# Kernel tuning notes

Hardware: AMD Instinct MI355X
Metric: run time of the kernel (lower is better)

## Reference

```python
import jax, jax.numpy as jnp
import numpy as np

NEG_INF = jnp.float32(-9e15)

def gat_layer(x, adj_mask, W, a, alpha):
    # x: [N, F_in]; W: [H, F_in, F_out]; a: [H, 2*F_out]; adj_mask: [N, N] bool
    H, _, O = W.shape
    h = jnp.einsum('nf,hfo->hno', x, W)            # [H, N, O]
    a_src, a_dst = a[:, :O], a[:, O:]              # [H, O] each
    e_src = jnp.einsum('hno,ho->hn', h, a_src)     # [H, N]
    e_dst = jnp.einsum('hno,ho->hn', h, a_dst)     # [H, N]
    e = jax.nn.leaky_relu(e_src[:, :, None] + e_dst[:, None, :], negative_slope=alpha)
    e = jnp.where(adj_mask[None, :, :], e, NEG_INF)  # mask non-edges
    attn = jax.nn.softmax(e, axis=-1)              # [H, N, N]
    out = jnp.einsum('hnm,hmo->hno', attn, h)      # [H, N, O]
    return out.mean(axis=0)                        # average heads -> [N, O]

def setup_inputs() -> dict:
    key = jax.random.key(0)
    ks = jax.random.split(key, 6)
    N, F_IN, F_HID, F_CLS, H = 4096, 512, 256, 16, 4
    x = jax.random.normal(ks[0], (N, F_IN), dtype=jnp.float32)
    adj = jax.random.randint(ks[1], (N, N), 0, 2, dtype=jnp.int32)
    W1 = jax.random.normal(ks[2], (H, F_IN, F_HID), dtype=jnp.float32) * 0.05
    a1 = jax.random.normal(ks[3], (H, 2 * F_HID), dtype=jnp.float32) * 0.05
    W2 = jax.random.normal(ks[4], (1, F_HID, F_CLS), dtype=jnp.float32) * 0.05
    a2 = jax.random.normal(ks[5], (1, 2 * F_CLS), dtype=jnp.float32) * 0.05
    return {"x": x, "adj": adj, "W1": W1, "a1": a1, "W2": W2, "a2": a2}

def reference(x, adj, W1, a1, W2, a2):
    alpha = 0.2
    adj_mask = adj > 0
    h = jax.nn.relu(gat_layer(x, adj_mask, W1, a1, alpha))        # layer1 + ReLU
    out = gat_layer(h, adj_mask, W2, a2, alpha)                    # layer2
    return jax.nn.log_softmax(out, axis=1)                         # [N, nclass]
```

## Files before the change

### kernel.cpp

```cpp
#include <hip/hip_runtime.h>
#include <stdint.h>

#define N_NODES 4096
#define F_IN    512
#define F_HID   256
#define F_CLS   16
#define NHEAD   4
#define ALPHA   0.2f

typedef __attribute__((ext_vector_type(8))) short short8;
typedef __attribute__((ext_vector_type(4))) float f32x4;

__device__ __forceinline__ float bf2f(unsigned short h) {
    unsigned u = ((unsigned)h) << 16; float f; __builtin_memcpy(&f, &u, 4); return f;
}
__device__ __forceinline__ unsigned short f2bf(float f) {
    unsigned u; __builtin_memcpy(&u, &f, 4);
    u += 0x7fffu + ((u >> 16) & 1u);
    return (unsigned short)(u >> 16);
}
__device__ __forceinline__ float lo_bf(unsigned u) { u <<= 16;          float f; __builtin_memcpy(&f,&u,4); return f; }
__device__ __forceinline__ float hi_bf(unsigned u) { u &= 0xffff0000u;  float f; __builtin_memcpy(&f,&u,4); return f; }

__device__ __forceinline__ void async_cp16(void* lds, const void* g) {
    __builtin_amdgcn_global_load_lds(
        (const __attribute__((address_space(1))) unsigned int*)g,
        (__attribute__((address_space(3))) unsigned int*)lds,
        16, 0, 0);
}

__global__ __launch_bounds__(256) void k_bitmask(const int* __restrict__ adj,
                                                 unsigned long long* __restrict__ bm) {
    int wv = threadIdx.x >> 6, lane = threadIdx.x & 63;
    int idx0 = blockIdx.x * 1024 + wv * 256;
    const int* p = adj + idx0 + lane;
    unsigned long long m0 = __ballot(p[0]   > 0);
    unsigned long long m1 = __ballot(p[64]  > 0);
    unsigned long long m2 = __ballot(p[128] > 0);
    unsigned long long m3 = __ballot(p[192] > 0);
    if (lane == 0) {
        int w = idx0 >> 6;
        bm[w] = m0; bm[w+1] = m1; bm[w+2] = m2; bm[w+3] = m3;
    }
}

__global__ __launch_bounds__(256) void k_convert(const float* __restrict__ x,
                                                 const float* __restrict__ W1,
                                                 const float* __restrict__ W2,
                                                 unsigned short* __restrict__ xb,
                                                 unsigned short* __restrict__ W1t,
                                                 float* __restrict__ W2t) {
    int tid = blockIdx.x * 256 + threadIdx.x;
    const int NXV = (N_NODES * F_IN) / 8;
    const int NW1 = NHEAD * 64 * F_HID;
    if (tid < NXV) {
        float4 a = *(const float4*)&x[tid * 8];
        float4 b = *(const float4*)&x[tid * 8 + 4];
        uint4 w;
        w.x = (unsigned)f2bf(a.x) | ((unsigned)f2bf(a.y) << 16);
        w.y = (unsigned)f2bf(a.z) | ((unsigned)f2bf(a.w) << 16);
        w.z = (unsigned)f2bf(b.x) | ((unsigned)f2bf(b.y) << 16);
        w.w = (unsigned)f2bf(b.z) | ((unsigned)f2bf(b.w) << 16);
        *(uint4*)&xb[tid * 8] = w;
    } else if (tid < NXV + NW1) {
        int j = tid - NXV;
        int o = j & 255, f8 = (j >> 8) & 63, h = j >> 14;
        float v[8];
        #pragma unroll
        for (int k = 0; k < 8; ++k)
            v[k] = W1[(size_t)(h * F_IN + f8 * 8 + k) * F_HID + o];
        uint4 w;
        w.x = (unsigned)f2bf(v[0]) | ((unsigned)f2bf(v[1]) << 16);
        w.y = (unsigned)f2bf(v[2]) | ((unsigned)f2bf(v[3]) << 16);
        w.z = (unsigned)f2bf(v[4]) | ((unsigned)f2bf(v[5]) << 16);
        w.w = (unsigned)f2bf(v[6]) | ((unsigned)f2bf(v[7]) << 16);
        *(uint4*)&W1t[(size_t)(h * F_HID + o) * F_IN + f8 * 8] = w;
    } else {
        int j = tid - NXV - NW1;
        if (j < F_HID * F_CLS) {
            int o = j >> 4, c = j & 15;
            W2t[c * F_HID + o] = W2[j];
        }
    }
}

__global__ __launch_bounds__(256, 4) void k_gemm1(const unsigned short* __restrict__ xb,
                                                  const unsigned short* __restrict__ W1t,
                                                  const float* __restrict__ a1,
                                                  unsigned short* __restrict__ h1t,
                                                  float* __restrict__ es1,
                                                  float* __restrict__ ed1) {
    __shared__ unsigned short Ald[2][64 * 32];
    __shared__ unsigned short Bld[2][128 * 32];
    const int t = threadIdx.x;
    const int lane = t & 63, wv = t >> 6, quad = lane >> 4, l15 = lane & 15;
    const int wn = wv & 1, wo = wv >> 1;
    const int n0 = blockIdx.x * 128;
    const int mo0 = blockIdx.y * 64;
    const int h = blockIdx.z;

    {
        int chunk = wv * 64 + lane, row = chunk >> 2, ch = lane & 3;
        async_cp16(&Ald[0][wv * 512], W1t + (size_t)(h * F_HID + mo0 + row) * F_IN + ch * 8);
        #pragma unroll
        for (int ps = 0; ps < 2; ++ps) {
            int c2 = (wv * 2 + ps) * 64 + lane, r2 = c2 >> 2;
            async_cp16(&Bld[0][(wv * 2 + ps) * 512], xb + (size_t)(n0 + r2) * F_IN + ch * 8);
        }
    }
    f32x4 acc[2][4] = {};
    for (int it = 0; it < 16; ++it) {
        const int cur = it & 1;
        __syncthreads();
        if (it + 1 < 16) {
            const int k2 = (it + 1) * 32;
            int chunk = wv * 64 + lane, row = chunk >> 2, ch = lane & 3;
            async_cp16(&Ald[1 - cur][wv * 512], W1t + (size_t)(h * F_HID + mo0 + row) * F_IN + k2 + ch * 8);
            #pragma unroll
            for (int ps = 0; ps < 2; ++ps) {
                int c2 = (wv * 2 + ps) * 64 + lane, r2 = c2 >> 2;
                async_cp16(&Bld[1 - cur][(wv * 2 + ps) * 512], xb + (size_t)(n0 + r2) * F_IN + k2 + ch * 8);
            }
        }
        short8 bf[4];
        #pragma unroll
        for (int ni = 0; ni < 4; ++ni)
            bf[ni] = *(const short8*)&Bld[cur][(wn * 64 + ni * 16 + l15) * 32 + quad * 8];
        #pragma unroll
        for (int mi = 0; mi < 2; ++mi) {
            short8 af = *(const short8*)&Ald[cur][(wo * 32 + mi * 16 + l15) * 32 + quad * 8];
            #pragma unroll
            for (int ni = 0; ni < 4; ++ni)
                acc[mi][ni] = __builtin_amdgcn_mfma_f32_16x16x32_bf16(af, bf[ni], acc[mi][ni], 0, 0, 0);
        }
    }
    #pragma unroll
    for (int mi = 0; mi < 2; ++mi)
      #pragma unroll
      for (int ni = 0; ni < 4; ++ni)
        #pragma unroll
        for (int rg = 0; rg < 4; ++rg) {
            int o = mo0 + wo * 32 + mi * 16 + quad * 4 + rg;
            int n = n0 + wn * 64 + ni * 16 + l15;
            h1t[(size_t)(h * F_HID + o) * N_NODES + n] = f2bf(acc[mi][ni][rg]);
        }
    float esp[4] = {}, edp[4] = {};
    #pragma unroll
    for (int mi = 0; mi < 2; ++mi)
      #pragma unroll
      for (int rg = 0; rg < 4; ++rg) {
        int o = mo0 + wo * 32 + mi * 16 + quad * 4 + rg;
        float a1s = a1[h * 2 * F_HID + o];
        float a1d = a1[h * 2 * F_HID + F_HID + o];
        #pragma unroll
        for (int ni = 0; ni < 4; ++ni) {
            esp[ni] += acc[mi][ni][rg] * a1s;
            edp[ni] += acc[mi][ni][rg] * a1d;
        }
      }
    #pragma unroll
    for (int ni = 0; ni < 4; ++ni) {
        esp[ni] += __shfl_xor(esp[ni], 16, 64); esp[ni] += __shfl_xor(esp[ni], 32, 64);
        edp[ni] += __shfl_xor(edp[ni], 16, 64); edp[ni] += __shfl_xor(edp[ni], 32, 64);
    }
    if (quad == 0) {
        #pragma unroll
        for (int ni = 0; ni < 4; ++ni) {
            int n = n0 + wn * 64 + ni * 16 + l15;
            atomicAdd(&es1[h * N_NODES + n], esp[ni]);
            atomicAdd(&ed1[h * N_NODES + n], edp[ni]);
        }
    }
}

__global__ __launch_bounds__(512, 4) void k_attn1(const unsigned short* __restrict__ h1t,
                                                  const float* __restrict__ es1,
                                                  const float* __restrict__ ed1,
                                                  const unsigned char* __restrict__ bmb,
                                                  unsigned short* __restrict__ C1p,
                                                  float* __restrict__ l1p) {
    __shared__ unsigned short Bld[2][256 * 32];
    const int t = threadIdx.x;
    const int lane = t & 63, wv = t >> 6, quad = lane >> 4, l15 = lane & 15;
    const int wvo = wv & 1, wvm = wv >> 1;
    const int m0 = blockIdx.x * 128;
    const int h = blockIdx.y;
    const int kz = blockIdx.z;
    const int mb0 = kz * 1024;

    int m_r0 = m0 + wvm * 32 + l15;
    int m_r1 = m_r0 + 16;
    float esr0 = es1[h * N_NODES + m_r0];
    float esr1 = es1[h * N_NODES + m_r1];
    const unsigned char* bp0 = bmb + (size_t)m_r0 * (N_NODES / 8);
    const unsigned char* bp1 = bmb + (size_t)m_r1 * (N_NODES / 8);
    const float* edb = ed1 + h * N_NODES;

    {
        int ch = lane & 3;
        #pragma unroll
        for (int ps = 0; ps < 2; ++ps) {
            int row = ((wv * 2 + ps) * 64 + lane) >> 2;
            async_cp16(&Bld[0][(wv * 2 + ps) * 512], h1t + (size_t)(h * F_HID + row) * N_NODES + mb0 + ch * 8);
        }
    }
    f32x4 acc[8][2] = {};
    float lsum0 = 0.f, lsum1 = 0.f;
    for (int it = 0; it < 32; ++it) {
        const int cur = it & 1;
        const int mb = mb0 + it * 32;
        __syncthreads();
        if (it + 1 < 32) {
            int ch = lane & 3;
            #pragma unroll
            for (int ps = 0; ps < 2; ++ps) {
                int row = ((wv * 2 + ps) * 64 + lane) >> 2;
                async_cp16(&Bld[1 - cur][(wv * 2 + ps) * 512],
                           h1t + (size_t)(h * F_HID + row) * N_NODES + mb + 32 + ch * 8);
            }
        }
        float4 e0 = *(const float4*)&edb[mb + quad * 8];
        float4 e1v = *(const float4*)&edb[mb + quad * 8 + 4];
        float ev[8] = {e0.x, e0.y, e0.z, e0.w, e1v.x, e1v.y, e1v.z, e1v.w};
        unsigned bb0 = bp0[(mb >> 3) + quad];
        unsigned bb1 = bp1[(mb >> 3) + quad];
        short8 bfrag0, bfrag1;
        #pragma unroll
        for (int j = 0; j < 8; ++j) {
            float s0 = esr0 + ev[j]; s0 = fmaxf(s0, ALPHA * s0);
            float p0 = ((bb0 >> j) & 1u) ? __expf(s0) : 0.f;
            lsum0 += p0; bfrag0[j] = (short)f2bf(p0);
            float s1 = esr1 + ev[j]; s1 = fmaxf(s1, ALPHA * s1);
            float p1 = ((bb1 >> j) & 1u) ? __expf(s1) : 0.f;
            lsum1 += p1; bfrag1[j] = (short)f2bf(p1);
        }
        #pragma unroll
        for (int mi = 0; mi < 8; ++mi) {
            short8 af = *(const short8*)&Bld[cur][(wvo * 128 + mi * 16 + l15) * 32 + quad * 8];
            acc[mi][0] = __builtin_amdgcn_mfma_f32_16x16x32_bf16(af, bfrag0, acc[mi][0], 0, 0, 0);
            acc[mi][1] = __builtin_amdgcn_mfma_f32_16x16x32_bf16(af, bfrag1, acc[mi][1], 0, 0, 0);
        }
    }
    lsum0 += __shfl_xor(lsum0, 16, 64); lsum0 += __shfl_xor(lsum0, 32, 64);
    lsum1 += __shfl_xor(lsum1, 16, 64); lsum1 += __shfl_xor(lsum1, 32, 64);
    if (quad == 0 && wvo == 0) {
        l1p[(size_t)(kz * NHEAD + h) * N_NODES + m_r0] = lsum0;
        l1p[(size_t)(kz * NHEAD + h) * N_NODES + m_r1] = lsum1;
    }
    unsigned short* Cb = C1p + (size_t)(kz * NHEAD + h) * N_NODES * F_HID;
    #pragma unroll
    for (int mi = 0; mi < 8; ++mi)
      #pragma unroll
      for (int ni = 0; ni < 2; ++ni) {
        int o0 = wvo * 128 + mi * 16 + quad * 4;
        int m = (ni == 0) ? m_r0 : m_r1;
        uint2 uu;
        uu.x = (unsigned)f2bf(acc[mi][ni][0]) | ((unsigned)f2bf(acc[mi][ni][1]) << 16);
        uu.y = (unsigned)f2bf(acc[mi][ni][2]) | ((unsigned)f2bf(acc[mi][ni][3]) << 16);
        *(uint2*)&Cb[(size_t)m * F_HID + o0] = uu;
      }
}

__global__ __launch_bounds__(256) void k_reduce1(const unsigned short* __restrict__ C1p,
                                                 const float* __restrict__ l1p,
                                                 unsigned short* __restrict__ h2) {
    int t = threadIdx.x;
    int og = t & 31, nl = t >> 5;
    int n = blockIdx.x * 8 + nl;
    float acc8[8] = {};
    #pragma unroll
    for (int h = 0; h < NHEAD; ++h) {
        float den = 0.f, num[8] = {};
        #pragma unroll
        for (int kz = 0; kz < 4; ++kz) {
            den += l1p[(size_t)(kz * NHEAD + h) * N_NODES + n];
            uint4 u = *(const uint4*)&C1p[((size_t)(kz * NHEAD + h) * N_NODES + n) * F_HID + og * 8];
            num[0] += lo_bf(u.x); num[1] += hi_bf(u.x);
            num[2] += lo_bf(u.y); num[3] += hi_bf(u.y);
            num[4] += lo_bf(u.z); num[5] += hi_bf(u.z);
            num[6] += lo_bf(u.w); num[7] += hi_bf(u.w);
        }
        float rinv = 1.f / fmaxf(den, 1e-30f);
        #pragma unroll
        for (int j = 0; j < 8; ++j) acc8[j] += num[j] * rinv;
    }
    uint4 w;
    unsigned short b[8];
    #pragma unroll
    for (int j = 0; j < 8; ++j) b[j] = f2bf(fmaxf(acc8[j] * 0.25f, 0.f));
    w.x = (unsigned)b[0] | ((unsigned)b[1] << 16);
    w.y = (unsigned)b[2] | ((unsigned)b[3] << 16);
    w.z = (unsigned)b[4] | ((unsigned)b[5] << 16);
    w.w = (unsigned)b[6] | ((unsigned)b[7] << 16);
    *(uint4*)&h2[(size_t)n * F_HID + og * 8] = w;
}

__global__ __launch_bounds__(256) void k_h2w(const unsigned short* __restrict__ h2,
                                             const float* __restrict__ W2t,
                                             const float* __restrict__ a2,
                                             unsigned short* __restrict__ h2wt,
                                             float* __restrict__ es2, float* __restrict__ ed2) {
    int t = threadIdx.x;
    int c = t & 15, nl = t >> 4;
    int n = blockIdx.x * 16 + nl;
    const unsigned short* hrow = h2 + (size_t)n * F_HID;
    const float* wrow = W2t + c * F_HID;
    float dot = 0.f;
    for (int o = 0; o < F_HID; o += 8) {
        uint4 hu = *(const uint4*)&hrow[o];
        float4 w0 = *(const float4*)&wrow[o];
        float4 w1 = *(const float4*)&wrow[o + 4];
        dot += lo_bf(hu.x)*w0.x + hi_bf(hu.x)*w0.y + lo_bf(hu.y)*w0.z + hi_bf(hu.y)*w0.w;
        dot += lo_bf(hu.z)*w1.x + hi_bf(hu.z)*w1.y + lo_bf(hu.w)*w1.z + hi_bf(hu.w)*w1.w;
    }
    h2wt[(size_t)c * N_NODES + n] = f2bf(dot);
    float es = dot * a2[c];
    float ed = dot * a2[F_CLS + c];
    #pragma unroll
    for (int off = 1; off < 16; off <<= 1) {
        es += __shfl_xor(es, off, 64);
        ed += __shfl_xor(ed, off, 64);
    }
    if (c == 0) { es2[n] = es; ed2[n] = ed; }
}

__global__ __launch_bounds__(256, 4) void k_attn2(const unsigned short* __restrict__ h2wt,
                                                  const float* __restrict__ es2,
                                                  const float* __restrict__ ed2,
                                                  const unsigned char* __restrict__ bmb,
                                                  float* __restrict__ out2p,
                                                  float* __restrict__ l2p) {
    const int t = threadIdx.x;
    const int lane = t & 63, wv = t >> 6, quad = lane >> 4, l15 = lane & 15;
    const int m0 = blockIdx.x * 64;
    const int ks = blockIdx.y;
    const int m_r = m0 + wv * 16 + l15;
    const float esr = es2[m_r];
    const unsigned char* bp = bmb + (size_t)m_r * (N_NODES / 8);

    f32x4 acc = {};
    float lsum = 0.f;
    for (int it = 0; it < 16; ++it) {
        const int mb = ks * 512 + it * 32;
        float4 e0 = *(const float4*)&ed2[mb + quad * 8];
        float4 e1v = *(const float4*)&ed2[mb + quad * 8 + 4];
        float ev[8] = {e0.x, e0.y, e0.z, e0.w, e1v.x, e1v.y, e1v.z, e1v.w};
        unsigned bb = bp[(mb >> 3) + quad];
        short8 afrag;
        #pragma unroll
        for (int j = 0; j < 8; ++j) {
            float s = esr + ev[j]; s = fmaxf(s, ALPHA * s);
            float p = ((bb >> j) & 1u) ? __expf(s) : 0.f;
            lsum += p; afrag[j] = (short)f2bf(p);
        }
        short8 bfr = *(const short8*)&h2wt[(size_t)l15 * N_NODES + mb + quad * 8];
        acc = __builtin_amdgcn_mfma_f32_16x16x32_bf16(afrag, bfr, acc, 0, 0, 0);
    }
    lsum += __shfl_xor(lsum, 16, 64); lsum += __shfl_xor(lsum, 32, 64);
    if (quad == 0) l2p[(size_t)ks * N_NODES + m_r] = lsum;
    #pragma unroll
    for (int rg = 0; rg < 4; ++rg) {
        int row = m0 + wv * 16 + quad * 4 + rg;
        out2p[((size_t)ks * N_NODES + row) * F_CLS + l15] = acc[rg];
    }
}

__global__ __launch_bounds__(256) void k_final(const float* __restrict__ out2p,
                                               const float* __restrict__ l2p,
                                               float* __restrict__ out) {
    int t = threadIdx.x;
    int c = t & 15, nl = t >> 4;
    int n = blockIdx.x * 16 + nl;
    float v = 0.f, l = 0.f;
    #pragma unroll
    for (int ks = 0; ks < 8; ++ks) {
        v += out2p[((size_t)ks * N_NODES + n) * F_CLS + c];
        l += l2p[(size_t)ks * N_NODES + n];
    }
    v /= fmaxf(l, 1e-30f);
    float mx = v;
    #pragma unroll
    for (int off = 1; off < 16; off <<= 1) mx = fmaxf(mx, __shfl_xor(mx, off, 64));
    float e = __expf(v - mx);
    float se = e;
    #pragma unroll
    for (int off = 1; off < 16; off <<= 1) se += __shfl_xor(se, off, 64);
    out[(size_t)n * F_CLS + c] = v - mx - __logf(se);
}

#define OFF_BM    0ull
#define OFF_XB    2097152ull
#define OFF_W1T   6291456ull
#define OFF_W2T   7340032ull
#define OFF_ES1   7356416ull
#define OFF_ED1   7421952ull
#define OFF_ES2   7487488ull
#define OFF_ED2   7503872ull
#define OFF_L1P   7520256ull
#define OFF_L2P   7782400ull
#define OFF_H2    7910400ull
#define OFF_OUT2P 7910400ull
#define OFF_H2WT  10007552ull
#define OFF_H1T   10138624ull
#define OFF_C1P   18527232ull

extern "C" void kernel_launch(void* const* d_in, const int* in_sizes, int n_in,
                              void* d_out, int out_size, void* d_ws, size_t ws_size,
                              hipStream_t stream) {
    const float* x   = (const float*)d_in[0];
    const int*   adj = (const int*)d_in[1];
    const float* W1  = (const float*)d_in[2];
    const float* a1  = (const float*)d_in[3];
    const float* W2  = (const float*)d_in[4];
    const float* a2  = (const float*)d_in[5];
    float* out = (float*)d_out;
    char* ws = (char*)d_ws;

    unsigned long long* bm  = (unsigned long long*)(ws + OFF_BM);
    unsigned char*      bmb = (unsigned char*)(ws + OFF_BM);
    unsigned short* xb   = (unsigned short*)(ws + OFF_XB);
    unsigned short* W1t  = (unsigned short*)(ws + OFF_W1T);
    float* W2t   = (float*)(ws + OFF_W2T);
    float* es1   = (float*)(ws + OFF_ES1);
    float* ed1   = (float*)(ws + OFF_ED1);
    float* es2   = (float*)(ws + OFF_ES2);
    float* ed2   = (float*)(ws + OFF_ED2);
    float* l1p   = (float*)(ws + OFF_L1P);
    float* l2p   = (float*)(ws + OFF_L2P);
    unsigned short* h2   = (unsigned short*)(ws + OFF_H2);
    float* out2p = (float*)(ws + OFF_OUT2P);
    unsigned short* h2wt = (unsigned short*)(ws + OFF_H2WT);
    unsigned short* h1t  = (unsigned short*)(ws + OFF_H1T);
    unsigned short* C1p  = (unsigned short*)(ws + OFF_C1P);

    hipMemsetAsync(es1, 0, 131072, stream);
    k_bitmask <<<dim3(16384),    256, 0, stream>>>(adj, bm);
    k_convert <<<dim3(1296),     256, 0, stream>>>(x, W1, W2, xb, W1t, W2t);
    k_gemm1   <<<dim3(32, 4, 4), 256, 0, stream>>>(xb, W1t, a1, h1t, es1, ed1);
    k_attn1   <<<dim3(32, 4, 4), 512, 0, stream>>>(h1t, es1, ed1, bmb, C1p, l1p);
    k_reduce1 <<<dim3(512),      256, 0, stream>>>(C1p, l1p, h2);
    k_h2w     <<<dim3(256),      256, 0, stream>>>(h2, W2t, a2, h2wt, es2, ed2);
    k_attn2   <<<dim3(64, 8),    256, 0, stream>>>(h2wt, es2, ed2, bmb, out2p, l2p);
    k_final   <<<dim3(256),      256, 0, stream>>>(out2p, l2p, out);
}
```

Baseline: 241.3 us.

## Fuse prep kernels, fold log2e into scores, retile gemm1 and attn1

```diff
diff --git a/kernel.cpp b/kernel.cpp
--- a/kernel.cpp
+++ b/kernel.cpp
@@ -7,6 +7,7 @@
 #define F_CLS   16
 #define NHEAD   4
 #define ALPHA   0.2f
+#define LOG2E   1.4426950408889634f
 
 typedef __attribute__((ext_vector_type(8))) short short8;
 typedef __attribute__((ext_vector_type(4))) float f32x4;
@@ -29,58 +30,74 @@
         16, 0, 0);
 }
 
-__global__ __launch_bounds__(256) void k_bitmask(const int* __restrict__ adj,
-                                                 unsigned long long* __restrict__ bm) {
-    int wv = threadIdx.x >> 6, lane = threadIdx.x & 63;
-    int idx0 = blockIdx.x * 1024 + wv * 256;
-    const int* p = adj + idx0 + lane;
-    unsigned long long m0 = __ballot(p[0]   > 0);
-    unsigned long long m1 = __ballot(p[64]  > 0);
-    unsigned long long m2 = __ballot(p[128] > 0);
-    unsigned long long m3 = __ballot(p[192] > 0);
-    if (lane == 0) {
-        int w = idx0 >> 6;
-        bm[w] = m0; bm[w+1] = m1; bm[w+2] = m2; bm[w+3] = m3;
-    }
-}
-
-__global__ __launch_bounds__(256) void k_convert(const float* __restrict__ x,
-                                                 const float* __restrict__ W1,
-                                                 const float* __restrict__ W2,
-                                                 unsigned short* __restrict__ xb,
-                                                 unsigned short* __restrict__ W1t,
-                                                 float* __restrict__ W2t) {
-    int tid = blockIdx.x * 256 + threadIdx.x;
-    const int NXV = (N_NODES * F_IN) / 8;
-    const int NW1 = NHEAD * 64 * F_HID;
-    if (tid < NXV) {
-        float4 a = *(const float4*)&x[tid * 8];
-        float4 b = *(const float4*)&x[tid * 8 + 4];
-        uint4 w;
-        w.x = (unsigned)f2bf(a.x) | ((unsigned)f2bf(a.y) << 16);
-        w.y = (unsigned)f2bf(a.z) | ((unsigned)f2bf(a.w) << 16);
-        w.z = (unsigned)f2bf(b.x) | ((unsigned)f2bf(b.y) << 16);
-        w.w = (unsigned)f2bf(b.z) | ((unsigned)f2bf(b.w) << 16);
-        *(uint4*)&xb[tid * 8] = w;
-    } else if (tid < NXV + NW1) {
-        int j = tid - NXV;
-        int o = j & 255, f8 = (j >> 8) & 63, h = j >> 14;
-        float v[8];
-        #pragma unroll
-        for (int k = 0; k < 8; ++k)
-            v[k] = W1[(size_t)(h * F_IN + f8 * 8 + k) * F_HID + o];
-        uint4 w;
-        w.x = (unsigned)f2bf(v[0]) | ((unsigned)f2bf(v[1]) << 16);
-        w.y = (unsigned)f2bf(v[2]) | ((unsigned)f2bf(v[3]) << 16);
-        w.z = (unsigned)f2bf(v[4]) | ((unsigned)f2bf(v[5]) << 16);
-        w.w = (unsigned)f2bf(v[6]) | ((unsigned)f2bf(v[7]) << 16);
-        *(uint4*)&W1t[(size_t)(h * F_HID + o) * F_IN + f8 * 8] = w;
-    } else {
-        int j = tid - NXV - NW1;
-        if (j < F_HID * F_CLS) {
-            int o = j >> 4, c = j & 15;
-            W2t[c * F_HID + o] = W2[j];
-        }
+#define PREP_BM_BLOCKS   16384
+#define PREP_CV_BLOCKS   1296
+#define PREP_Z_BLOCKS    4
+__global__ __launch_bounds__(256) void k_prep(const int* __restrict__ adj,
+                                              const float* __restrict__ x,
+                                              const float* __restrict__ W1,
+                                              const float* __restrict__ W2,
+                                              unsigned long long* __restrict__ bm,
+                                              unsigned short* __restrict__ xb,
+                                              unsigned short* __restrict__ W1t,
+                                              float* __restrict__ W2t,
+                                              float* __restrict__ ez) {
+    int b = blockIdx.x;
+    if (b < PREP_BM_BLOCKS) {
+        int wv = threadIdx.x >> 6, lane = threadIdx.x & 63;
+        int idx0 = b * 1024 + wv * 256;
+        const int* p = adj + idx0 + lane;
+        unsigned long long m0 = __ballot(p[0]   > 0);
+        unsigned long long m1 = __ballot(p[64]  > 0);
+        unsigned long long m2 = __ballot(p[128] > 0);
+        unsigned long long m3 = __ballot(p[192] > 0);
+        if (lane == 0) {
+            int w = idx0 >> 6;
+            bm[w] = m0; bm[w+1] = m1; bm[w+2] = m2; bm[w+3] = m3;
+        }
+        return;
+    }
+    if (b < PREP_BM_BLOCKS + PREP_CV_BLOCKS) {
+        int tid = (b - PREP_BM_BLOCKS) * 256 + threadIdx.x;
+        const int NXV = (N_NODES * F_IN) / 8;
+        const int NW1 = NHEAD * 64 * F_HID;
+        if (tid < NXV) {
+            float4 a = *(const float4*)&x[tid * 8];
+            float4 c = *(const float4*)&x[tid * 8 + 4];
+            uint4 w;
+            w.x = (unsigned)f2bf(a.x) | ((unsigned)f2bf(a.y) << 16);
+            w.y = (unsigned)f2bf(a.z) | ((unsigned)f2bf(a.w) << 16);
+            w.z = (unsigned)f2bf(c.x) | ((unsigned)f2bf(c.y) << 16);
+            w.w = (unsigned)f2bf(c.z) | ((unsigned)f2bf(c.w) << 16);
+            *(uint4*)&xb[tid * 8] = w;
+        } else if (tid < NXV + NW1) {
+            int j = tid - NXV;
+            int o = j & 255, f8 = (j >> 8) & 63, h = j >> 14;
+            float v[8];
+            #pragma unroll
+            for (int k = 0; k < 8; ++k)
+                v[k] = W1[(size_t)(h * F_IN + f8 * 8 + k) * F_HID + o];
+            uint4 w;
+            w.x = (unsigned)f2bf(v[0]) | ((unsigned)f2bf(v[1]) << 16);
+            w.y = (unsigned)f2bf(v[2]) | ((unsigned)f2bf(v[3]) << 16);
+            w.z = (unsigned)f2bf(v[4]) | ((unsigned)f2bf(v[5]) << 16);
+            w.w = (unsigned)f2bf(v[6]) | ((unsigned)f2bf(v[7]) << 16);
+            *(uint4*)&W1t[(size_t)(h * F_HID + o) * F_IN + f8 * 8] = w;
+        } else {
+            int j = tid - NXV - NW1;
+            if (j < F_HID * F_CLS) {
+                int o = j >> 4, c = j & 15;
+                W2t[c * F_HID + o] = W2[j];
+            }
+        }
+        return;
+    }
+    {
+        int zb = b - PREP_BM_BLOCKS - PREP_CV_BLOCKS;
+        float4* z4 = (float4*)ez;
+        #pragma unroll
+        for (int r = 0; r < 8; ++r)
+            z4[zb * 2048 + r * 256 + threadIdx.x] = make_float4(0.f, 0.f, 0.f, 0.f);
     }
 }
 
@@ -90,173 +107,175 @@
                                                   unsigned short* __restrict__ h1t,
                                                   float* __restrict__ es1,
                                                   float* __restrict__ ed1) {
-    __shared__ unsigned short Ald[2][64 * 32];
-    __shared__ unsigned short Bld[2][128 * 32];
+    __shared__ unsigned short Sld[2][6144];
     const int t = threadIdx.x;
     const int lane = t & 63, wv = t >> 6, quad = lane >> 4, l15 = lane & 15;
     const int wn = wv & 1, wo = wv >> 1;
     const int n0 = blockIdx.x * 128;
-    const int mo0 = blockIdx.y * 64;
+    const int oo0 = blockIdx.y * 64;
     const int h = blockIdx.z;
-
-    {
-        int chunk = wv * 64 + lane, row = chunk >> 2, ch = lane & 3;
-        async_cp16(&Ald[0][wv * 512], W1t + (size_t)(h * F_HID + mo0 + row) * F_IN + ch * 8);
-        #pragma unroll
-        for (int ps = 0; ps < 2; ++ps) {
-            int c2 = (wv * 2 + ps) * 64 + lane, r2 = c2 >> 2;
-            async_cp16(&Bld[0][(wv * 2 + ps) * 512], xb + (size_t)(n0 + r2) * F_IN + ch * 8);
-        }
-    }
-    f32x4 acc[2][4] = {};
+    const int kl = (lane >> 4) * 8;
+
+    const unsigned short* gs[3];
+    int loff[3];
+    #pragma unroll
+    for (int s = 0; s < 3; ++s) {
+        int c = wv * 3 + s;
+        loff[s] = c * 512;
+        gs[s] = (c < 8)
+            ? (xb  + (size_t)(n0 + c * 16 + l15) * F_IN + kl)
+            : (W1t + (size_t)(h * F_HID + oo0 + (c - 8) * 16 + l15) * F_IN + kl);
+    }
+    #pragma unroll
+    for (int s = 0; s < 3; ++s) async_cp16(&Sld[0][loff[s]], gs[s]);
+
+    f32x4 acc[4][2] = {};
     for (int it = 0; it < 16; ++it) {
         const int cur = it & 1;
         __syncthreads();
         if (it + 1 < 16) {
-            const int k2 = (it + 1) * 32;
-            int chunk = wv * 64 + lane, row = chunk >> 2, ch = lane & 3;
-            async_cp16(&Ald[1 - cur][wv * 512], W1t + (size_t)(h * F_HID + mo0 + row) * F_IN + k2 + ch * 8);
+            const int off = (it + 1) * 32;
             #pragma unroll
-            for (int ps = 0; ps < 2; ++ps) {
-                int c2 = (wv * 2 + ps) * 64 + lane, r2 = c2 >> 2;
-                async_cp16(&Bld[1 - cur][(wv * 2 + ps) * 512], xb + (size_t)(n0 + r2) * F_IN + k2 + ch * 8);
+            for (int s = 0; s < 3; ++s) async_cp16(&Sld[1 - cur][loff[s]], gs[s] + off);
+        }
+        short8 bfw[2];
+        #pragma unroll
+        for (int mi = 0; mi < 2; ++mi)
+            bfw[mi] = *(const short8*)&Sld[cur][(8 + wo * 2 + mi) * 512 + lane * 8];
+        #pragma unroll
+        for (int ni = 0; ni < 4; ++ni) {
+            short8 af = *(const short8*)&Sld[cur][(wn * 4 + ni) * 512 + lane * 8];
+            #pragma unroll
+            for (int mi = 0; mi < 2; ++mi)
+                acc[ni][mi] = __builtin_amdgcn_mfma_f32_16x16x32_bf16(af, bfw[mi], acc[ni][mi], 0, 0, 0);
+        }
+    }
+    #pragma unroll
+    for (int ni = 0; ni < 4; ++ni)
+      #pragma unroll
+      for (int mi = 0; mi < 2; ++mi) {
+        int o = oo0 + wo * 32 + mi * 16 + l15;
+        int nb = n0 + wn * 64 + ni * 16 + quad * 4;
+        uint2 uu;
+        uu.x = (unsigned)f2bf(acc[ni][mi][0]) | ((unsigned)f2bf(acc[ni][mi][1]) << 16);
+        uu.y = (unsigned)f2bf(acc[ni][mi][2]) | ((unsigned)f2bf(acc[ni][mi][3]) << 16);
+        *(uint2*)&h1t[(size_t)(h * F_HID + o) * N_NODES + nb] = uu;
+      }
+    float a1s[2], a1d[2];
+    #pragma unroll
+    for (int mi = 0; mi < 2; ++mi) {
+        int o = oo0 + wo * 32 + mi * 16 + l15;
+        a1s[mi] = a1[h * 2 * F_HID + o] * LOG2E;
+        a1d[mi] = a1[h * 2 * F_HID + F_HID + o] * LOG2E;
+    }
+    #pragma unroll
+    for (int ni = 0; ni < 4; ++ni) {
+        #pragma unroll
+        for (int rg = 0; rg < 4; ++rg) {
+            float es = acc[ni][0][rg] * a1s[0] + acc[ni][1][rg] * a1s[1];
+            float ed = acc[ni][0][rg] * a1d[0] + acc[ni][1][rg] * a1d[1];
+            #pragma unroll
+            for (int off = 1; off < 16; off <<= 1) {
+                es += __shfl_xor(es, off, 64);
+                ed += __shfl_xor(ed, off, 64);
             }
-        }
-        short8 bf[4];
-        #pragma unroll
-        for (int ni = 0; ni < 4; ++ni)
-            bf[ni] = *(const short8*)&Bld[cur][(wn * 64 + ni * 16 + l15) * 32 + quad * 8];
-        #pragma unroll
-        for (int mi = 0; mi < 2; ++mi) {
-            short8 af = *(const short8*)&Ald[cur][(wo * 32 + mi * 16 + l15) * 32 + quad * 8];
-            #pragma unroll
-            for (int ni = 0; ni < 4; ++ni)
-                acc[mi][ni] = __builtin_amdgcn_mfma_f32_16x16x32_bf16(af, bf[ni], acc[mi][ni], 0, 0, 0);
-        }
-    }
-    #pragma unroll
-    for (int mi = 0; mi < 2; ++mi)
-      #pragma unroll
-      for (int ni = 0; ni < 4; ++ni)
-        #pragma unroll
-        for (int rg = 0; rg < 4; ++rg) {
-            int o = mo0 + wo * 32 + mi * 16 + quad * 4 + rg;
-            int n = n0 + wn * 64 + ni * 16 + l15;
-            h1t[(size_t)(h * F_HID + o) * N_NODES + n] = f2bf(acc[mi][ni][rg]);
-        }
-    float esp[4] = {}, edp[4] = {};
-    #pragma unroll
-    for (int mi = 0; mi < 2; ++mi)
-      #pragma unroll
-      for (int rg = 0; rg < 4; ++rg) {
-        int o = mo0 + wo * 32 + mi * 16 + quad * 4 + rg;
-        float a1s = a1[h * 2 * F_HID + o];
-        float a1d = a1[h * 2 * F_HID + F_HID + o];
-        #pragma unroll
-        for (int ni = 0; ni < 4; ++ni) {
-            esp[ni] += acc[mi][ni][rg] * a1s;
-            edp[ni] += acc[mi][ni][rg] * a1d;
-        }
-      }
-    #pragma unroll
-    for (int ni = 0; ni < 4; ++ni) {
-        esp[ni] += __shfl_xor(esp[ni], 16, 64); esp[ni] += __shfl_xor(esp[ni], 32, 64);
-        edp[ni] += __shfl_xor(edp[ni], 16, 64); edp[ni] += __shfl_xor(edp[ni], 32, 64);
-    }
-    if (quad == 0) {
-        #pragma unroll
-        for (int ni = 0; ni < 4; ++ni) {
-            int n = n0 + wn * 64 + ni * 16 + l15;
-            atomicAdd(&es1[h * N_NODES + n], esp[ni]);
-            atomicAdd(&ed1[h * N_NODES + n], edp[ni]);
-        }
-    }
-}
-
-__global__ __launch_bounds__(512, 4) void k_attn1(const unsigned short* __restrict__ h1t,
+            if (l15 == 0) {
+                int n = n0 + wn * 64 + ni * 16 + quad * 4 + rg;
+                atomicAdd(&es1[h * N_NODES + n], es);
+                atomicAdd(&ed1[h * N_NODES + n], ed);
+            }
+        }
+    }
+}
+
+__global__ __launch_bounds__(512, 2) void k_attn1(const unsigned short* __restrict__ h1t,
                                                   const float* __restrict__ es1,
                                                   const float* __restrict__ ed1,
                                                   const unsigned char* __restrict__ bmb,
                                                   unsigned short* __restrict__ C1p,
                                                   float* __restrict__ l1p) {
-    __shared__ unsigned short Bld[2][256 * 32];
+    __shared__ unsigned short Bld[2][8192];
     const int t = threadIdx.x;
     const int lane = t & 63, wv = t >> 6, quad = lane >> 4, l15 = lane & 15;
-    const int wvo = wv & 1, wvm = wv >> 1;
-    const int m0 = blockIdx.x * 128;
+    const int m0 = blockIdx.x * 256;
     const int h = blockIdx.y;
     const int kz = blockIdx.z;
     const int mb0 = kz * 1024;
 
-    int m_r0 = m0 + wvm * 32 + l15;
-    int m_r1 = m_r0 + 16;
-    float esr0 = es1[h * N_NODES + m_r0];
-    float esr1 = es1[h * N_NODES + m_r1];
+    const int m_r0 = m0 + wv * 32 + l15;
+    const int m_r1 = m_r0 + 16;
+    const float esr0 = es1[h * N_NODES + m_r0];
+    const float esr1 = es1[h * N_NODES + m_r1];
     const unsigned char* bp0 = bmb + (size_t)m_r0 * (N_NODES / 8);
     const unsigned char* bp1 = bmb + (size_t)m_r1 * (N_NODES / 8);
     const float* edb = ed1 + h * N_NODES;
 
-    {
-        int ch = lane & 3;
-        #pragma unroll
-        for (int ps = 0; ps < 2; ++ps) {
-            int row = ((wv * 2 + ps) * 64 + lane) >> 2;
-            async_cp16(&Bld[0][(wv * 2 + ps) * 512], h1t + (size_t)(h * F_HID + row) * N_NODES + mb0 + ch * 8);
-        }
-    }
-    f32x4 acc[8][2] = {};
+    const unsigned short* gb0 = h1t + (size_t)(h * F_HID + wv * 16 + l15) * N_NODES + (lane >> 4) * 8;
+    const unsigned short* gb1 = h1t + (size_t)(h * F_HID + (wv + 8) * 16 + l15) * N_NODES + (lane >> 4) * 8;
+    async_cp16(&Bld[0][wv * 512], gb0 + mb0);
+    async_cp16(&Bld[0][(wv + 8) * 512], gb1 + mb0);
+
+    f32x4 acc[16][2] = {};
     float lsum0 = 0.f, lsum1 = 0.f;
     for (int it = 0; it < 32; ++it) {
         const int cur = it & 1;
         const int mb = mb0 + it * 32;
         __syncthreads();
         if (it + 1 < 32) {
-            int ch = lane & 3;
-            #pragma unroll
-            for (int ps = 0; ps < 2; ++ps) {
-                int row = ((wv * 2 + ps) * 64 + lane) >> 2;
-                async_cp16(&Bld[1 - cur][(wv * 2 + ps) * 512],
-                           h1t + (size_t)(h * F_HID + row) * N_NODES + mb + 32 + ch * 8);
-            }
+            async_cp16(&Bld[1 - cur][wv * 512], gb0 + mb + 32);
+            async_cp16(&Bld[1 - cur][(wv + 8) * 512], gb1 + mb + 32);
         }
         float4 e0 = *(const float4*)&edb[mb + quad * 8];
         float4 e1v = *(const float4*)&edb[mb + quad * 8 + 4];
         float ev[8] = {e0.x, e0.y, e0.z, e0.w, e1v.x, e1v.y, e1v.z, e1v.w};
         unsigned bb0 = bp0[(mb >> 3) + quad];
         unsigned bb1 = bp1[(mb >> 3) + quad];
-        short8 bfrag0, bfrag1;
+        unsigned up0[8], up1[8];
         #pragma unroll
         for (int j = 0; j < 8; ++j) {
             float s0 = esr0 + ev[j]; s0 = fmaxf(s0, ALPHA * s0);
-            float p0 = ((bb0 >> j) & 1u) ? __expf(s0) : 0.f;
-            lsum0 += p0; bfrag0[j] = (short)f2bf(p0);
+            float p0 = ((bb0 >> j) & 1u) ? __builtin_amdgcn_exp2f(s0) : 0.f;
+            unsigned u0; __builtin_memcpy(&u0, &p0, 4); u0 &= 0xffff0000u;
+            float pt0; __builtin_memcpy(&pt0, &u0, 4);
+            lsum0 += pt0; up0[j] = u0;
             float s1 = esr1 + ev[j]; s1 = fmaxf(s1, ALPHA * s1);
-            float p1 = ((bb1 >> j) & 1u) ? __expf(s1) : 0.f;
-            lsum1 += p1; bfrag1[j] = (short)f2bf(p1);
-        }
-        #pragma unroll
-        for (int mi = 0; mi < 8; ++mi) {
-            short8 af = *(const short8*)&Bld[cur][(wvo * 128 + mi * 16 + l15) * 32 + quad * 8];
-            acc[mi][0] = __builtin_amdgcn_mfma_f32_16x16x32_bf16(af, bfrag0, acc[mi][0], 0, 0, 0);
-            acc[mi][1] = __builtin_amdgcn_mfma_f32_16x16x32_bf16(af, bfrag1, acc[mi][1], 0, 0, 0);
+            float p1 = ((bb1 >> j) & 1u) ? __builtin_amdgcn_exp2f(s1) : 0.f;
+            unsigned u1; __builtin_memcpy(&u1, &p1, 4); u1 &= 0xffff0000u;
+            float pt1; __builtin_memcpy(&pt1, &u1, 4);
+            lsum1 += pt1; up1[j] = u1;
+        }
+        int pk0[4], pk1[4];
+        #pragma unroll
+        for (int j = 0; j < 4; ++j) {
+            pk0[j] = __builtin_amdgcn_perm(up0[2*j+1], up0[2*j], 0x07060302u);
+            pk1[j] = __builtin_amdgcn_perm(up1[2*j+1], up1[2*j], 0x07060302u);
+        }
+        short8 bfrag0, bfrag1;
+        __builtin_memcpy(&bfrag0, pk0, 16);
+        __builtin_memcpy(&bfrag1, pk1, 16);
+        #pragma unroll
+        for (int ot = 0; ot < 16; ++ot) {
+            short8 af = *(const short8*)&Bld[cur][ot * 512 + lane * 8];
+            acc[ot][0] = __builtin_amdgcn_mfma_f32_16x16x32_bf16(af, bfrag0, acc[ot][0], 0, 0, 0);
+            acc[ot][1] = __builtin_amdgcn_mfma_f32_16x16x32_bf16(af, bfrag1, acc[ot][1], 0, 0, 0);
         }
     }
     lsum0 += __shfl_xor(lsum0, 16, 64); lsum0 += __shfl_xor(lsum0, 32, 64);
     lsum1 += __shfl_xor(lsum1, 16, 64); lsum1 += __shfl_xor(lsum1, 32, 64);
-    if (quad == 0 && wvo == 0) {
+    if (quad == 0) {
         l1p[(size_t)(kz * NHEAD + h) * N_NODES + m_r0] = lsum0;
         l1p[(size_t)(kz * NHEAD + h) * N_NODES + m_r1] = lsum1;
     }
     unsigned short* Cb = C1p + (size_t)(kz * NHEAD + h) * N_NODES * F_HID;
     #pragma unroll
-    for (int mi = 0; mi < 8; ++mi)
+    for (int ot = 0; ot < 16; ++ot)
       #pragma unroll
-      for (int ni = 0; ni < 2; ++ni) {
-        int o0 = wvo * 128 + mi * 16 + quad * 4;
-        int m = (ni == 0) ? m_r0 : m_r1;
+      for (int mi = 0; mi < 2; ++mi) {
+        int m = (mi == 0) ? m_r0 : m_r1;
+        int o0 = ot * 16 + quad * 4;
         uint2 uu;
-        uu.x = (unsigned)f2bf(acc[mi][ni][0]) | ((unsigned)f2bf(acc[mi][ni][1]) << 16);
-        uu.y = (unsigned)f2bf(acc[mi][ni][2]) | ((unsigned)f2bf(acc[mi][ni][3]) << 16);
+        uu.x = (unsigned)f2bf(acc[ot][mi][0]) | ((unsigned)f2bf(acc[ot][mi][1]) << 16);
+        uu.y = (unsigned)f2bf(acc[ot][mi][2]) | ((unsigned)f2bf(acc[ot][mi][3]) << 16);
         *(uint2*)&Cb[(size_t)m * F_HID + o0] = uu;
       }
 }
@@ -285,13 +304,13 @@
         for (int j = 0; j < 8; ++j) acc8[j] += num[j] * rinv;
     }
     uint4 w;
-    unsigned short b[8];
-    #pragma unroll
-    for (int j = 0; j < 8; ++j) b[j] = f2bf(fmaxf(acc8[j] * 0.25f, 0.f));
-    w.x = (unsigned)b[0] | ((unsigned)b[1] << 16);
-    w.y = (unsigned)b[2] | ((unsigned)b[3] << 16);
-    w.z = (unsigned)b[4] | ((unsigned)b[5] << 16);
-    w.w = (unsigned)b[6] | ((unsigned)b[7] << 16);
+    unsigned short bq[8];
+    #pragma unroll
+    for (int j = 0; j < 8; ++j) bq[j] = f2bf(fmaxf(acc8[j] * 0.25f, 0.f));
+    w.x = (unsigned)bq[0] | ((unsigned)bq[1] << 16);
+    w.y = (unsigned)bq[2] | ((unsigned)bq[3] << 16);
+    w.z = (unsigned)bq[4] | ((unsigned)bq[5] << 16);
+    w.w = (unsigned)bq[6] | ((unsigned)bq[7] << 16);
     *(uint4*)&h2[(size_t)n * F_HID + og * 8] = w;
 }
 
@@ -314,8 +333,8 @@
         dot += lo_bf(hu.z)*w1.x + hi_bf(hu.z)*w1.y + lo_bf(hu.w)*w1.z + hi_bf(hu.w)*w1.w;
     }
     h2wt[(size_t)c * N_NODES + n] = f2bf(dot);
-    float es = dot * a2[c];
-    float ed = dot * a2[F_CLS + c];
+    float es = dot * a2[c] * LOG2E;
+    float ed = dot * a2[F_CLS + c] * LOG2E;
     #pragma unroll
     for (int off = 1; off < 16; off <<= 1) {
         es += __shfl_xor(es, off, 64);
@@ -350,7 +369,7 @@
         #pragma unroll
         for (int j = 0; j < 8; ++j) {
             float s = esr + ev[j]; s = fmaxf(s, ALPHA * s);
-            float p = ((bb >> j) & 1u) ? __expf(s) : 0.f;
+            float p = ((bb >> j) & 1u) ? __builtin_amdgcn_exp2f(s) : 0.f;
             lsum += p; afrag[j] = (short)f2bf(p);
         }
         short8 bfr = *(const short8*)&h2wt[(size_t)l15 * N_NODES + mb + quad * 8];
@@ -433,11 +452,10 @@
     unsigned short* h1t  = (unsigned short*)(ws + OFF_H1T);
     unsigned short* C1p  = (unsigned short*)(ws + OFF_C1P);
 
-    hipMemsetAsync(es1, 0, 131072, stream);
-    k_bitmask <<<dim3(16384),    256, 0, stream>>>(adj, bm);
-    k_convert <<<dim3(1296),     256, 0, stream>>>(x, W1, W2, xb, W1t, W2t);
+    k_prep    <<<dim3(PREP_BM_BLOCKS + PREP_CV_BLOCKS + PREP_Z_BLOCKS), 256, 0, stream>>>(
+                  adj, x, W1, W2, bm, xb, W1t, W2t, es1);
     k_gemm1   <<<dim3(32, 4, 4), 256, 0, stream>>>(xb, W1t, a1, h1t, es1, ed1);
-    k_attn1   <<<dim3(32, 4, 4), 512, 0, stream>>>(h1t, es1, ed1, bmb, C1p, l1p);
+    k_attn1   <<<dim3(16, 4, 4), 512, 0, stream>>>(h1t, es1, ed1, bmb, C1p, l1p);
     k_reduce1 <<<dim3(512),      256, 0, stream>>>(C1p, l1p, h2);
     k_h2w     <<<dim3(256),      256, 0, stream>>>(h2, W2t, a2, h2wt, es2, ed2);
     k_attn2   <<<dim3(64, 8),    256, 0, stream>>>(h2wt, es2, ed2, bmb, out2p, l2p);
```

New measurement: 232.4 us. 1.04x faster.
